# Kernel tuning notes

Hardware: AMD Instinct MI355X
Metric: run time of the kernel (lower is better)

## Reference

```python
import jax, jax.numpy as jnp
import numpy as np

K = 3          # kernel_size
STRIDE = 1
ITERS = 3      # num_iterations


def _squash(t, axis=-1):
    sn = jnp.sum(t * t, axis=axis, keepdims=True)
    return sn / (1.0 + sn) * t / jnp.sqrt(sn)


def setup_inputs() -> dict:
    key = jax.random.key(0)
    k1, k2 = jax.random.split(key)
    x = jax.random.normal(k1, (4, 32, 14, 14, 8), dtype=jnp.float32)
    # route_weights: [num_capsules, num_in_capsules*K*K, in_channels, out_channels]
    route_weights = jax.random.normal(k2, (32, 32 * K * K, 8, 16), dtype=jnp.float32)
    bias = jnp.zeros((32, 16), dtype=jnp.float32)  # torch init fills with 0.0
    return {"x": x, "route_weights": route_weights, "bias": bias}


def reference(x, route_weights, bias):
    B, Ci, H, W_, Cin = x.shape
    A, N, _, D = route_weights.shape  # num_capsules, route_nodes, in_ch, out_ch
    w = (H - K) // STRIDE + 1
    # Extract all KxK windows at once. idx: [w, K]
    idx = jnp.arange(w)[:, None] * STRIDE + jnp.arange(K)[None, :]
    # xw: [B, Ci, w, K, w, K, Cin]
    xw = x[:, :, idx[:, :, None, None], idx[None, None, :, :], :]
    # -> [B, w, w, Ci*K*K, Cin]; node ordering (Ci, K, K) matches torch .view
    xw = xw.transpose(0, 2, 4, 1, 3, 5, 6).reshape(B, w, w, Ci * K * K, Cin)
    # priors: [A, B, w, w, N, D]
    priors = jnp.einsum('bijnc,ancd->abijnd', xw, route_weights)
    # logits broadcast over D in the original (delta has trailing dim 1),
    # so keep them as scalars per route node: [A, B, w, w, N]
    logits = jnp.zeros((A, B, w, w, N), dtype=priors.dtype)
    b = bias[:, None, None, None, :]  # [A,1,1,1,D]
    out = None
    for i in range(ITERS):
        probs = jax.nn.softmax(logits, axis=-1)  # softmax over route nodes (dim=2 in torch)
        s = jnp.einsum('abijn,abijnd->abijd', probs, priors) + b
        out = _squash(s)
        if i != ITERS - 1:
            logits = logits + jnp.einsum('abijnd,abijd->abijn', priors, out)
    # torch permutes (num_caps, B, w, w, D) -> (B, num_caps, w, w, D)
    return out.transpose(1, 0, 2, 3, 4)
```

## Files before the change

kernel.cpp:

```cpp
#include <hip/hip_runtime.h>

#define W_OUT 12
#define N_CAPS 288
#define CIN 8
#define DD 16
#define A_DIM 32
#define B_DIM 4
#define CI 32
#define H_IN 14
#define NT 18
#define XSTRIDE 9
#define NROWS 576

__device__ __forceinline__ float4 shfl_xor4(float4 v, int m) {
    float4 r;
    r.x = __shfl_xor(v.x, m);
    r.y = __shfl_xor(v.y, m);
    r.z = __shfl_xor(v.z, m);
    r.w = __shfl_xor(v.w, m);
    return r;
}

__global__ __launch_bounds__(256, 4) void capsule_kernel(
    const float* __restrict__ x,
    const float* __restrict__ Wt,
    const float* __restrict__ bias,
    float* __restrict__ out)
{
    __shared__ float xs[NROWS * XSTRIDE];
    __shared__ int   xoff[N_CAPS];

    const int tid = threadIdx.x;
    int bid = blockIdx.x;
    const int jb = bid % 3; bid /= 3;
    const int i  = bid % W_OUT; bid /= W_OUT;
    const int b  = bid % B_DIM; bid /= B_DIM;
    const int a  = bid;
    const int j0 = jb * 4;

    for (int n = tid; n < N_CAPS; n += 256) {
        int ci = n / 9, r = n % 9;
        xoff[n] = (ci * 18 + (r / 3) * 6 + (r % 3)) * XSTRIDE;
    }

    for (int row = tid; row < NROWS; row += 256) {
        int ci = row / 18, rr = row % 18;
        int ki = rr / 6, jj = rr % 6;
        const float* src = x + ((((size_t)b * CI + ci) * H_IN + (i + ki)) * H_IN + (j0 + jj)) * CIN;
        float4 v0 = *reinterpret_cast<const float4*>(src);
        float4 v1 = *reinterpret_cast<const float4*>(src + 4);
        float* dst = &xs[row * XSTRIDE];
        dst[0] = v0.x; dst[1] = v0.y; dst[2] = v0.z; dst[3] = v0.w;
        dst[4] = v1.x; dst[5] = v1.y; dst[6] = v1.z; dst[7] = v1.w;
    }
    __syncthreads();

    const int lane = tid & 63;
    const int sj   = tid >> 6;
    const int dq   = lane & 3;
    const int nr   = lane >> 2;

    const float* Wa = Wt + (size_t)a * (N_CAPS * CIN * DD);
    const int sjoff = sj * XSTRIDE;

    float4 ps[NT];
    #pragma unroll
    for (int t = 0; t < NT; ++t) {
        const int n = nr + 16 * t;
        const float* wp = Wa + (size_t)n * (CIN * DD) + dq * 4;
        const float* xp = &xs[xoff[n] + sjoff];
        float4 acc = {0.f, 0.f, 0.f, 0.f};
        #pragma unroll
        for (int c = 0; c < CIN; ++c) {
            float4 w4 = *reinterpret_cast<const float4*>(wp + c * DD);
            float xv = xp[c];
            acc.x = fmaf(xv, w4.x, acc.x);
            acc.y = fmaf(xv, w4.y, acc.y);
            acc.z = fmaf(xv, w4.z, acc.z);
            acc.w = fmaf(xv, w4.w, acc.w);
        }
        ps[t] = acc;
        __builtin_amdgcn_sched_barrier(0);
    }

    const float4 bv = *reinterpret_cast<const float4*>(bias + a * DD + dq * 4);

    float lt[NT];
    float4 out4;

    {
        float4 s = {0.f, 0.f, 0.f, 0.f};
        #pragma unroll
        for (int t = 0; t < NT; ++t) {
            s.x += ps[t].x; s.y += ps[t].y; s.z += ps[t].z; s.w += ps[t].w;
        }
        #pragma unroll
        for (int m = 4; m <= 32; m <<= 1) { float4 o = shfl_xor4(s, m); s.x += o.x; s.y += o.y; s.z += o.z; s.w += o.w; }
        const float inv0 = 1.0f / 288.0f;
        s.x = fmaf(s.x, inv0, bv.x); s.y = fmaf(s.y, inv0, bv.y);
        s.z = fmaf(s.z, inv0, bv.z); s.w = fmaf(s.w, inv0, bv.w);
        float sn = s.x*s.x + s.y*s.y + s.z*s.z + s.w*s.w;
        sn += __shfl_xor(sn, 1); sn += __shfl_xor(sn, 2);
        float factor = sn / (1.0f + sn) * rsqrtf(sn);
        out4.x = factor * s.x; out4.y = factor * s.y; out4.z = factor * s.z; out4.w = factor * s.w;

        #pragma unroll
        for (int t = 0; t < NT; ++t) {
            float p = ps[t].x*out4.x + ps[t].y*out4.y + ps[t].z*out4.z + ps[t].w*out4.w;
            p += __shfl_xor(p, 1);
            p += __shfl_xor(p, 2);
            lt[t] = p;
        }
    }

    #pragma unroll
    for (int it = 1; it < 3; ++it) {
        float m = -1e30f;
        #pragma unroll
        for (int t = 0; t < NT; ++t) m = fmaxf(m, lt[t]);
        #pragma unroll
        for (int msk = 4; msk <= 32; msk <<= 1) m = fmaxf(m, __shfl_xor(m, msk));
        float se = 0.f;
        #pragma unroll
        for (int t = 0; t < NT; ++t) se += __expf(lt[t] - m);
        #pragma unroll
        for (int msk = 4; msk <= 32; msk <<= 1) se += __shfl_xor(se, msk);
        const float inv = 1.0f / se;

        float4 s = {0.f, 0.f, 0.f, 0.f};
        #pragma unroll
        for (int t = 0; t < NT; ++t) {
            float e = __expf(lt[t] - m);
            s.x = fmaf(e, ps[t].x, s.x); s.y = fmaf(e, ps[t].y, s.y);
            s.z = fmaf(e, ps[t].z, s.z); s.w = fmaf(e, ps[t].w, s.w);
        }
        #pragma unroll
        for (int msk = 4; msk <= 32; msk <<= 1) { float4 o = shfl_xor4(s, msk); s.x += o.x; s.y += o.y; s.z += o.z; s.w += o.w; }
        s.x = fmaf(s.x, inv, bv.x); s.y = fmaf(s.y, inv, bv.y);
        s.z = fmaf(s.z, inv, bv.z); s.w = fmaf(s.w, inv, bv.w);

        float sn = s.x*s.x + s.y*s.y + s.z*s.z + s.w*s.w;
        sn += __shfl_xor(sn, 1); sn += __shfl_xor(sn, 2);
        float factor = sn / (1.0f + sn) * rsqrtf(sn);
        out4.x = factor * s.x; out4.y = factor * s.y; out4.z = factor * s.z; out4.w = factor * s.w;

        if (it != 2) {
            #pragma unroll
            for (int t = 0; t < NT; ++t) {
                float p = ps[t].x*out4.x + ps[t].y*out4.y + ps[t].z*out4.z + ps[t].w*out4.w;
                p += __shfl_xor(p, 1);
                p += __shfl_xor(p, 2);
                lt[t] += p;
            }
        }
    }

    if (nr == 0) {
        size_t o = ((((size_t)b * A_DIM + a) * W_OUT + i) * W_OUT + (j0 + sj)) * DD + dq * 4;
        *reinterpret_cast<float4*>(out + o) = out4;
    }
}

extern "C" void kernel_launch(void* const* d_in, const int* in_sizes, int n_in,
                              void* d_out, int out_size, void* d_ws, size_t ws_size,
                              hipStream_t stream) {
    const float* x    = (const float*)d_in[0];
    const float* Wt   = (const float*)d_in[1];
    const float* bias = (const float*)d_in[2];
    float* out = (float*)d_out;
    (void)in_sizes; (void)n_in; (void)out_size; (void)d_ws; (void)ws_size;

    const int grid = A_DIM * B_DIM * W_OUT * 3;
    capsule_kernel<<<grid, 256, 0, stream>>>(x, Wt, bias, out);
}
```

Baseline: 142.2 us.

## Double-buffer weight loads in registers and vectorize shared-memory x reads

```diff
diff --git a/kernel.cpp b/kernel.cpp
--- a/kernel.cpp
+++ b/kernel.cpp
@@ -9,7 +9,7 @@
 #define CI 32
 #define H_IN 14
 #define NT 18
-#define XSTRIDE 9
+#define XSTRIDE 12
 #define NROWS 576
 
 __device__ __forceinline__ float4 shfl_xor4(float4 v, int m) {
@@ -21,14 +21,24 @@
     return r;
 }
 
-__global__ __launch_bounds__(256, 4) void capsule_kernel(
+__device__ __forceinline__ void fma8(float4& acc, const float* xr, const float4* wv) {
+    #pragma unroll
+    for (int c = 0; c < CIN; ++c) {
+        acc.x = fmaf(xr[c], wv[c].x, acc.x);
+        acc.y = fmaf(xr[c], wv[c].y, acc.y);
+        acc.z = fmaf(xr[c], wv[c].z, acc.z);
+        acc.w = fmaf(xr[c], wv[c].w, acc.w);
+    }
+}
+
+__global__ __launch_bounds__(256, 3) void capsule_kernel(
     const float* __restrict__ x,
     const float* __restrict__ Wt,
     const float* __restrict__ bias,
     float* __restrict__ out)
 {
-    __shared__ float xs[NROWS * XSTRIDE];
-    __shared__ int   xoff[N_CAPS];
+    __shared__ __align__(16) float xs[NROWS * XSTRIDE];
+    __shared__ int xoff[N_CAPS];
 
     const int tid = threadIdx.x;
     int bid = blockIdx.x;
@@ -50,8 +60,8 @@
         float4 v0 = *reinterpret_cast<const float4*>(src);
         float4 v1 = *reinterpret_cast<const float4*>(src + 4);
         float* dst = &xs[row * XSTRIDE];
-        dst[0] = v0.x; dst[1] = v0.y; dst[2] = v0.z; dst[3] = v0.w;
-        dst[4] = v1.x; dst[5] = v1.y; dst[6] = v1.z; dst[7] = v1.w;
+        *reinterpret_cast<float4*>(dst)     = v0;
+        *reinterpret_cast<float4*>(dst + 4) = v1;
     }
     __syncthreads();
 
@@ -64,22 +74,43 @@
     const int sjoff = sj * XSTRIDE;
 
     float4 ps[NT];
+    float4 wA[CIN], wB[CIN];
+    {
+        const float* wp0 = Wa + (size_t)nr * (CIN * DD) + dq * 4;
+        #pragma unroll
+        for (int c = 0; c < CIN; ++c) wA[c] = *reinterpret_cast<const float4*>(wp0 + c * DD);
+    }
     #pragma unroll
-    for (int t = 0; t < NT; ++t) {
-        const int n = nr + 16 * t;
-        const float* wp = Wa + (size_t)n * (CIN * DD) + dq * 4;
-        const float* xp = &xs[xoff[n] + sjoff];
-        float4 acc = {0.f, 0.f, 0.f, 0.f};
-        #pragma unroll
-        for (int c = 0; c < CIN; ++c) {
-            float4 w4 = *reinterpret_cast<const float4*>(wp + c * DD);
-            float xv = xp[c];
-            acc.x = fmaf(xv, w4.x, acc.x);
-            acc.y = fmaf(xv, w4.y, acc.y);
-            acc.z = fmaf(xv, w4.z, acc.z);
-            acc.w = fmaf(xv, w4.w, acc.w);
-        }
-        ps[t] = acc;
+    for (int tt = 0; tt < NT; tt += 2) {
+        {
+            const float* wp = Wa + (size_t)(nr + 16 * (tt + 1)) * (CIN * DD) + dq * 4;
+            #pragma unroll
+            for (int c = 0; c < CIN; ++c) wB[c] = *reinterpret_cast<const float4*>(wp + c * DD);
+        }
+        {
+            const float* xp = &xs[xoff[nr + 16 * tt] + sjoff];
+            float xr[CIN];
+            *reinterpret_cast<float4*>(&xr[0]) = *reinterpret_cast<const float4*>(xp);
+            *reinterpret_cast<float4*>(&xr[4]) = *reinterpret_cast<const float4*>(xp + 4);
+            float4 acc = {0.f, 0.f, 0.f, 0.f};
+            fma8(acc, xr, wA);
+            ps[tt] = acc;
+        }
+        __builtin_amdgcn_sched_barrier(0);
+        if (tt + 2 < NT) {
+            const float* wp = Wa + (size_t)(nr + 16 * (tt + 2)) * (CIN * DD) + dq * 4;
+            #pragma unroll
+            for (int c = 0; c < CIN; ++c) wA[c] = *reinterpret_cast<const float4*>(wp + c * DD);
+        }
+        {
+            const float* xp = &xs[xoff[nr + 16 * (tt + 1)] + sjoff];
+            float xr[CIN];
+            *reinterpret_cast<float4*>(&xr[0]) = *reinterpret_cast<const float4*>(xp);
+            *reinterpret_cast<float4*>(&xr[4]) = *reinterpret_cast<const float4*>(xp + 4);
+            float4 acc = {0.f, 0.f, 0.f, 0.f};
+            fma8(acc, xr, wB);
+            ps[tt + 1] = acc;
+        }
         __builtin_amdgcn_sched_barrier(0);
     }
 
@@ -120,9 +151,10 @@
         for (int t = 0; t < NT; ++t) m = fmaxf(m, lt[t]);
         #pragma unroll
         for (int msk = 4; msk <= 32; msk <<= 1) m = fmaxf(m, __shfl_xor(m, msk));
+        float e[NT];
         float se = 0.f;
         #pragma unroll
-        for (int t = 0; t < NT; ++t) se += __expf(lt[t] - m);
+        for (int t = 0; t < NT; ++t) { e[t] = __expf(lt[t] - m); se += e[t]; }
         #pragma unroll
         for (int msk = 4; msk <= 32; msk <<= 1) se += __shfl_xor(se, msk);
         const float inv = 1.0f / se;
@@ -130,9 +162,8 @@
         float4 s = {0.f, 0.f, 0.f, 0.f};
         #pragma unroll
         for (int t = 0; t < NT; ++t) {
-            float e = __expf(lt[t] - m);
-            s.x = fmaf(e, ps[t].x, s.x); s.y = fmaf(e, ps[t].y, s.y);
-            s.z = fmaf(e, ps[t].z, s.z); s.w = fmaf(e, ps[t].w, s.w);
+            s.x = fmaf(e[t], ps[t].x, s.x); s.y = fmaf(e[t], ps[t].y, s.y);
+            s.z = fmaf(e[t], ps[t].z, s.z); s.w = fmaf(e[t], ps[t].w, s.w);
         }
         #pragma unroll
         for (int msk = 4; msk <= 32; msk <<= 1) { float4 o = shfl_xor4(s, msk); s.x += o.x; s.y += o.y; s.z += o.z; s.w += o.w; }
```

Result: no change. 142.1 us (-0.1%).

## Stage route weights through double-buffered LDS with async global_load_lds

Applied to the files above, without the earlier changes.

```diff
diff --git a/kernel.cpp b/kernel.cpp
--- a/kernel.cpp
+++ b/kernel.cpp
@@ -9,8 +9,9 @@
 #define CI 32
 #define H_IN 14
 #define NT 18
-#define XSTRIDE 9
+#define XSTRIDE 12
 #define NROWS 576
+#define WCHUNK 2048
 
 __device__ __forceinline__ float4 shfl_xor4(float4 v, int m) {
     float4 r;
@@ -21,14 +22,21 @@
     return r;
 }
 
-__global__ __launch_bounds__(256, 4) void capsule_kernel(
+__device__ __forceinline__ void stage_piece(const float* g, float* lds) {
+    __builtin_amdgcn_global_load_lds(
+        (const __attribute__((address_space(1))) void*)g,
+        (__attribute__((address_space(3))) void*)lds, 16, 0, 0);
+}
+
+__global__ __launch_bounds__(256, 3) void capsule_kernel(
     const float* __restrict__ x,
     const float* __restrict__ Wt,
     const float* __restrict__ bias,
     float* __restrict__ out)
 {
-    __shared__ float xs[NROWS * XSTRIDE];
-    __shared__ int   xoff[N_CAPS];
+    __shared__ __align__(16) float xs[NROWS * XSTRIDE];
+    __shared__ __align__(16) float wbuf[2][WCHUNK];
+    __shared__ int xoff[N_CAPS];
 
     const int tid = threadIdx.x;
     int bid = blockIdx.x;
@@ -38,10 +46,31 @@
     const int a  = bid;
     const int j0 = jb * 4;
 
+    const int lane = tid & 63;
+    const int wv   = tid >> 6;
+    const int dq   = lane & 3;
+    const int nr   = lane >> 2;
+    const int swz  = nr & 7;
+
+    const float* Wa = Wt + (size_t)a * (N_CAPS * CIN * DD);
+
+    auto issue_stage = [&](int t, int buf) {
+        #pragma unroll
+        for (int k = 0; k < 2; ++k) {
+            int p  = wv * 2 + k;
+            int L  = p * 64 + lane;
+            int nl = L >> 5;
+            int G  = (L & ~31) | ((L & 31) ^ (nl & 7));
+            stage_piece(Wa + (size_t)t * WCHUNK + (size_t)G * 4, &wbuf[buf][p * 256]);
+        }
+    };
+
     for (int n = tid; n < N_CAPS; n += 256) {
         int ci = n / 9, r = n % 9;
         xoff[n] = (ci * 18 + (r / 3) * 6 + (r % 3)) * XSTRIDE;
     }
+
+    issue_stage(0, 0);
 
     for (int row = tid; row < NROWS; row += 256) {
         int ci = row / 18, rr = row % 18;
@@ -50,40 +79,47 @@
         float4 v0 = *reinterpret_cast<const float4*>(src);
         float4 v1 = *reinterpret_cast<const float4*>(src + 4);
         float* dst = &xs[row * XSTRIDE];
-        dst[0] = v0.x; dst[1] = v0.y; dst[2] = v0.z; dst[3] = v0.w;
-        dst[4] = v1.x; dst[5] = v1.y; dst[6] = v1.z; dst[7] = v1.w;
-    }
+        *reinterpret_cast<float4*>(dst)     = v0;
+        *reinterpret_cast<float4*>(dst + 4) = v1;
+    }
+    const float4 bv = *reinterpret_cast<const float4*>(bias + a * DD + dq * 4);
     __syncthreads();
-
-    const int lane = tid & 63;
-    const int sj   = tid >> 6;
-    const int dq   = lane & 3;
-    const int nr   = lane >> 2;
-
-    const float* Wa = Wt + (size_t)a * (N_CAPS * CIN * DD);
-    const int sjoff = sj * XSTRIDE;
+    issue_stage(1, 1);
+
+    const int sjoff = wv * XSTRIDE;
 
     float4 ps[NT];
     #pragma unroll
     for (int t = 0; t < NT; ++t) {
+        if (t < NT - 1) { asm volatile("s_waitcnt vmcnt(2)" ::: "memory"); }
+        else            { asm volatile("s_waitcnt vmcnt(0)" ::: "memory"); }
+        __builtin_amdgcn_sched_barrier(0);
+        __builtin_amdgcn_s_barrier();
+        __builtin_amdgcn_sched_barrier(0);
+
         const int n = nr + 16 * t;
-        const float* wp = Wa + (size_t)n * (CIN * DD) + dq * 4;
         const float* xp = &xs[xoff[n] + sjoff];
+        float xr[CIN];
+        *reinterpret_cast<float4*>(&xr[0]) = *reinterpret_cast<const float4*>(xp);
+        *reinterpret_cast<float4*>(&xr[4]) = *reinterpret_cast<const float4*>(xp + 4);
+
+        const float4* wb = reinterpret_cast<const float4*>(&wbuf[t & 1][0]);
         float4 acc = {0.f, 0.f, 0.f, 0.f};
         #pragma unroll
         for (int c = 0; c < CIN; ++c) {
-            float4 w4 = *reinterpret_cast<const float4*>(wp + c * DD);
-            float xv = xp[c];
-            acc.x = fmaf(xv, w4.x, acc.x);
-            acc.y = fmaf(xv, w4.y, acc.y);
-            acc.z = fmaf(xv, w4.z, acc.z);
-            acc.w = fmaf(xv, w4.w, acc.w);
+            float4 w4 = wb[nr * 32 + (((c << 2) | dq) ^ swz)];
+            acc.x = fmaf(xr[c], w4.x, acc.x);
+            acc.y = fmaf(xr[c], w4.y, acc.y);
+            acc.z = fmaf(xr[c], w4.z, acc.z);
+            acc.w = fmaf(xr[c], w4.w, acc.w);
         }
         ps[t] = acc;
-        __builtin_amdgcn_sched_barrier(0);
-    }
-
-    const float4 bv = *reinterpret_cast<const float4*>(bias + a * DD + dq * 4);
+
+        __builtin_amdgcn_sched_barrier(0);
+        __builtin_amdgcn_s_barrier();
+        __builtin_amdgcn_sched_barrier(0);
+        if (t + 2 < NT) issue_stage(t + 2, t & 1);
+    }
 
     float lt[NT];
     float4 out4;
@@ -120,9 +156,10 @@
         for (int t = 0; t < NT; ++t) m = fmaxf(m, lt[t]);
         #pragma unroll
         for (int msk = 4; msk <= 32; msk <<= 1) m = fmaxf(m, __shfl_xor(m, msk));
+        float e[NT];
         float se = 0.f;
         #pragma unroll
-        for (int t = 0; t < NT; ++t) se += __expf(lt[t] - m);
+        for (int t = 0; t < NT; ++t) { e[t] = __expf(lt[t] - m); se += e[t]; }
         #pragma unroll
         for (int msk = 4; msk <= 32; msk <<= 1) se += __shfl_xor(se, msk);
         const float inv = 1.0f / se;
@@ -130,9 +167,8 @@
         float4 s = {0.f, 0.f, 0.f, 0.f};
         #pragma unroll
         for (int t = 0; t < NT; ++t) {
-            float e = __expf(lt[t] - m);
-            s.x = fmaf(e, ps[t].x, s.x); s.y = fmaf(e, ps[t].y, s.y);
-            s.z = fmaf(e, ps[t].z, s.z); s.w = fmaf(e, ps[t].w, s.w);
+            s.x = fmaf(e[t], ps[t].x, s.x); s.y = fmaf(e[t], ps[t].y, s.y);
+            s.z = fmaf(e[t], ps[t].z, s.z); s.w = fmaf(e[t], ps[t].w, s.w);
         }
         #pragma unroll
         for (int msk = 4; msk <= 32; msk <<= 1) { float4 o = shfl_xor4(s, msk); s.x += o.x; s.y += o.y; s.z += o.z; s.w += o.w; }
@@ -156,7 +192,7 @@
     }
 
     if (nr == 0) {
-        size_t o = ((((size_t)b * A_DIM + a) * W_OUT + i) * W_OUT + (j0 + sj)) * DD + dq * 4;
+        size_t o = ((((size_t)b * A_DIM + a) * W_OUT + i) * W_OUT + (j0 + wv)) * DD + dq * 4;
         *reinterpret_cast<float4*>(out + o) = out4;
     }
 }
```

Measured after the change: 155.4 us. 9.3% more time.
